# Kernel optimization log

Measured on AMD Instinct MI355X. Metric: run time of the kernel, lower is better.

The kernel has to match this reference:

```python
import jax, jax.numpy as jnp
import numpy as np

N_NODES = 100000
N_EDGES = 640000
IN_DIM = 128
HID_DIM = 256
N_CLASS = 40
K = 3  # propagation steps


def setup_inputs() -> dict:
    key = jax.random.key(0)
    ks = jax.random.split(key, 5)
    feats = jax.random.normal(ks[0], (N_NODES, IN_DIM), dtype=jnp.float32)
    src = jax.random.randint(ks[1], (N_EDGES,), 0, N_NODES, dtype=jnp.int32)
    dst = jax.random.randint(ks[2], (N_EDGES,), 0, N_NODES, dtype=jnp.int32)
    W1 = jax.random.normal(ks[3], (IN_DIM, HID_DIM), dtype=jnp.float32) * (1.0 / np.sqrt(IN_DIM))
    b1 = jnp.zeros((HID_DIM,), dtype=jnp.float32)
    W2 = jax.random.normal(ks[4], (HID_DIM, N_CLASS), dtype=jnp.float32) * (1.0 / np.sqrt(HID_DIM))
    b2 = jnp.zeros((N_CLASS,), dtype=jnp.float32)
    return {"feats": feats, "src": src, "dst": dst, "W1": W1, "b1": b1, "W2": W2, "b2": b2}


def _grand_conv(feats, src, dst, order):
    # symmetric normalization: norm = in_deg^{-1/2} (clamped at 1)
    deg = jax.ops.segment_sum(jnp.ones_like(dst, dtype=feats.dtype), dst, num_segments=N_NODES)
    norm = jnp.clip(deg, 1.0) ** -0.5  # [N]
    w = (norm[src] * norm[dst])[:, None]  # [E, 1] edge weights (u_mul_v)
    x = feats
    y = feats
    for _ in range(order):
        # u_mul_e gather-multiply, then scatter-sum into dst (SpMM)
        x = jax.ops.segment_sum(x[src] * w, dst, num_segments=N_NODES)
        y = y + x
    return y / (order + 1)


def reference(feats, src, dst, W1, b1, W2, b2):
    h = _grand_conv(feats, src, dst, K)           # [N, IN_DIM]
    h = jax.nn.relu(h @ W1 + b1)                  # [N, HID_DIM]
    logits = h @ W2 + b2                          # [N, N_CLASS]
    return jax.nn.log_softmax(logits, axis=-1)
```

## Files before the change

### kernel.cpp

```cpp
#include <hip/hip_runtime.h>

#define NN 100000
#define NE 640000
#define IND 128
#define HD 256
#define NC 40
#define MT 64
#define HPAD 264
#define LPAD 52
#define NB 196
#define CAP 5120
#define EPB 2500
#define SGRID 2048

typedef unsigned short u16;
typedef unsigned int u32;
typedef __attribute__((ext_vector_type(8))) short bf16x8;
typedef __attribute__((ext_vector_type(4))) float f32x4;

__device__ __forceinline__ float bf2f(u16 u) {
    union { u32 i; float f; } c; c.i = ((u32)u) << 16; return c.f;
}
__device__ __forceinline__ u16 f2bf(float f) {
    union { float f; u32 i; } c; c.f = f;
    u32 i = c.i;
    return (u16)((i + 0x7FFFu + ((i >> 16) & 1u)) >> 16);
}
__device__ __forceinline__ float rfl_f(float v) {
    return __int_as_float(__builtin_amdgcn_readfirstlane(__float_as_int(v)));
}
__device__ __forceinline__ int wave_incl_scan(int v, int lane) {
    #pragma unroll
    for (int off = 1; off < 64; off <<= 1) {
        int t = __shfl_up(v, off);
        if (lane >= off) v += t;
    }
    return v;
}

__global__ __launch_bounds__(256) void prep_k(
    const float* __restrict__ W1, const float* __restrict__ W2,
    u16* __restrict__ pw1, u16* __restrict__ pw2)
{
    const int gtid = blockIdx.x * 256 + threadIdx.x;
    if (gtid < 4096) {
        int lane = gtid & 63, fid = gtid >> 6;
        int ks = fid & 3, ct = fid >> 2;
        int quad = lane >> 4, m = lane & 15;
        int n = ct * 16 + m;
        u16* o = pw1 + (size_t)gtid * 8;
        #pragma unroll
        for (int j = 0; j < 8; j++) o[j] = f2bf(W1[(ks * 32 + quad * 8 + j) * HD + n]);
    } else if (gtid < 4096 + 1536) {
        int idx = gtid - 4096;
        int lane = idx & 63, fid = idx >> 6;
        int ks = fid & 7, ct = fid >> 3;
        int quad = lane >> 4, m = lane & 15;
        int n = ct * 16 + m;
        u16* o = pw2 + (size_t)idx * 8;
        #pragma unroll
        for (int j = 0; j < 8; j++)
            o[j] = (n < NC) ? f2bf(W2[(ks * 32 + quad * 8 + j) * NC + n]) : (u16)0;
    }
}

__global__ __launch_bounds__(256) void bin_k(
    const int* __restrict__ src, const int* __restrict__ dst,
    int* __restrict__ gcur, u32* __restrict__ ebuf)
{
    __shared__ int cnt[NB], cur[NB], rdest[NB];
    __shared__ u32 vals[EPB];
    const int tid = threadIdx.x;
    const int e0 = blockIdx.x * EPB;

    if (tid < NB) cnt[tid] = 0;
    __syncthreads();
    for (int i = tid; i < EPB; i += 256)
        atomicAdd(&cnt[dst[e0 + i] >> 9], 1);
    __syncthreads();
    if (tid < 64) {
        int carry = 0;
        #pragma unroll
        for (int c = 0; c < 4; c++) {
            const int idx = c * 64 + tid;
            const int v = (idx < NB) ? cnt[idx] : 0;
            const int incl = wave_incl_scan(v, tid);
            if (idx < NB) cur[idx] = carry + incl - v;
            carry += __shfl(incl, 63);
        }
    }
    __syncthreads();
    for (int i = tid; i < EPB; i += 256) {
        const int s = src[e0 + i], d = dst[e0 + i];
        const int b = d >> 9;
        const int slot = atomicAdd(&cur[b], 1);
        vals[slot] = ((u32)(d & 511) << 17) | (u32)s;
    }
    __syncthreads();
    if (tid < NB) {
        const int c = cnt[tid];
        int st = 0;
        if (c > 0) st = atomicAdd(&gcur[tid], c);
        rdest[tid] = (st + c <= CAP) ? st : -1;
    }
    __syncthreads();
    if (tid < NB) {
        const int c = cnt[tid];
        const int st = rdest[tid];
        if (c > 0 && st >= 0) {
            const int lo = cur[tid] - c;
            u32* o = ebuf + (size_t)tid * CAP + st;
            for (int k = 0; k < c; k++) o[k] = vals[lo + k];
        }
    }
}

__global__ __launch_bounds__(256) void build_k(
    const int* __restrict__ gcur, u32* __restrict__ ebuf,
    int2* __restrict__ rb, float* __restrict__ norm, float* __restrict__ invn)
{
    __shared__ int rowcnt[512], rowoff[512], csum[8];
    __shared__ u32 evals[CAP];
    const int tid = threadIdx.x;
    const int b = blockIdx.x;
    const int bB = b * CAP;
    const int r0 = b * 512;
    const int nb = min(__builtin_amdgcn_readfirstlane(gcur[b]), CAP);

    rowcnt[tid] = 0; rowcnt[256 + tid] = 0;
    __syncthreads();
    for (int i = tid; i < nb; i += 256) {
        const u32 v = ebuf[bB + i];
        evals[i] = v;
        atomicAdd(&rowcnt[(v >> 17) & 511], 1);
    }
    __syncthreads();
    {
        const int w = tid >> 6, lane = tid & 63;
        #pragma unroll
        for (int r = 0; r < 2; r++) {
            const int c = r * 4 + w;
            const int v = rowcnt[c * 64 + lane];
            const int incl = wave_incl_scan(v, lane);
            rowoff[c * 64 + lane] = incl - v;
            if (lane == 63) csum[c] = incl;
        }
        __syncthreads();
        if (tid == 0) {
            int run = 0;
            #pragma unroll
            for (int c = 0; c < 8; c++) { const int t = csum[c]; csum[c] = run; run += t; }
        }
        __syncthreads();
        #pragma unroll
        for (int r = 0; r < 2; r++) {
            const int c = r * 4 + w;
            rowoff[c * 64 + lane] += csum[c];
        }
    }
    __syncthreads();
    #pragma unroll
    for (int r = 0; r < 2; r++) {
        const int idx = r * 256 + tid;
        const int row = r0 + idx;
        if (row < NN) {
            const int deg = rowcnt[idx];
            const int base = bB + rowoff[idx];
            rb[row] = make_int2(base, base + deg);
            const float dc = fmaxf((float)deg, 1.0f);
            norm[row] = rsqrtf(dc);
            invn[row] = sqrtf(dc);
        }
    }
    __syncthreads();
    for (int i = tid; i < nb; i += 256) {
        const u32 v = evals[i];
        const int rl = (v >> 17) & 511;
        const int pos = atomicAdd(&rowoff[rl], 1);
        ebuf[bB + pos] = v & 0x1FFFFu;
    }
}

__global__ __launch_bounds__(256) void conv_k(
    const float4* __restrict__ feats4, const float* __restrict__ norm,
    uint2* __restrict__ zF2, uint2* __restrict__ zA2, uint2* __restrict__ zB2)
{
    const int gtid = blockIdx.x * 256 + threadIdx.x, gsz = gridDim.x * 256;
    if (gtid < 96) {
        const int which = gtid >> 5, idx = gtid & 31;
        uint2* b = (which == 0) ? zF2 : (which == 1) ? zA2 : zB2;
        b[(size_t)NN * 32 + idx] = make_uint2(0u, 0u);
    }
    for (int i = gtid; i < NN * (IND / 4); i += gsz) {
        const float4 v = feats4[i];
        const float n = norm[i >> 5];
        uint2 o;
        o.x = (u32)f2bf(v.x * n) | ((u32)f2bf(v.y * n) << 16);
        o.y = (u32)f2bf(v.z * n) | ((u32)f2bf(v.w * n) << 16);
        zF2[i] = o;
    }
}

template <int LAST>
__global__ __launch_bounds__(256) void spmm_k(
    const u32* __restrict__ x, u32* __restrict__ xnext,
    const u32* __restrict__ x0, const u32* __restrict__ x1,
    const int2* __restrict__ rb, const int* __restrict__ csr,
    const float* __restrict__ norm, const float* __restrict__ invn)
{
    const int lane = threadIdx.x & 63;
    int wid = (blockIdx.x * 256 + threadIdx.x) >> 6;
    wid = __builtin_amdgcn_readfirstlane(wid);
    const int nw = SGRID * 4;

    for (int row = wid; row < NN; row += nw) {
        const int2 be = rb[row];
        const int beg = __builtin_amdgcn_readfirstlane(be.x);
        const int end = __builtin_amdgcn_readfirstlane(be.y);
        const float n = rfl_f(norm[row]);

        float a0 = 0.f, a1 = 0.f;
        for (int b = beg; b < end; b += 8) {
            int sN[8];
            #pragma unroll
            for (int j = 0; j < 8; j++) {
                const int ee = b + j;
                const int c = csr[ee];
                int s = __builtin_amdgcn_readfirstlane(c);
                if (ee >= end) s = NN;
                sN[j] = s;
            }
            u32 u[8];
            #pragma unroll
            for (int j = 0; j < 8; j++) {
                const u32* rp = x + ((size_t)sN[j] << 6);
                u[j] = rp[lane];
            }
            #pragma unroll
            for (int j = 0; j < 8; j++) {
                a0 += __int_as_float((int)(u[j] << 16));
                a1 += __int_as_float((int)(u[j] & 0xFFFF0000u));
            }
        }

        const size_t ri = (size_t)row * 64 + lane;
        u32 o;
        if (!LAST) {
            const float n2 = n * n;
            o = (u32)f2bf(a0 * n2) | ((u32)f2bf(a1 * n2) << 16);
        } else {
            const float inv = rfl_f(invn[row]);
            const u32 v0 = x0[ri];
            const u32 v1 = x1[ri];
            const u32 v2 = x[ri];
            const float s0 = (bf2f((u16)(v0 & 0xFFFFu)) + bf2f((u16)(v1 & 0xFFFFu))
                            + bf2f((u16)(v2 & 0xFFFFu))) * inv + a0 * n;
            const float s1 = (bf2f((u16)(v0 >> 16)) + bf2f((u16)(v1 >> 16))
                            + bf2f((u16)(v2 >> 16))) * inv + a1 * n;
            o = (u32)f2bf(s0 * 0.25f) | ((u32)f2bf(s1 * 0.25f) << 16);
        }
        xnext[ri] = o;
    }
}

__global__ __launch_bounds__(256, 4) void mlp_mfma_k(
    const u16* __restrict__ ys, const u16* __restrict__ pw1,
    const float* __restrict__ B1, const u16* __restrict__ pw2,
    const float* __restrict__ B2, float* __restrict__ out, int N)
{
    __shared__ __align__(16) u16 h_s[MT * HPAD];
    const int t = threadIdx.x;
    const int w = t >> 6, lane = t & 63;
    const int quad = lane >> 4, m = lane & 15;
    const int node0 = blockIdx.x * MT;
    float* const lw = (float*)((char*)h_s + (size_t)w * 16 * HPAD * 2);

    bf16x8 av[4][4];
    #pragma unroll
    for (int g = 0; g < 4; g++) {
        int node = node0 + g * 16 + m;
        if (node > N - 1) node = N - 1;
        #pragma unroll
        for (int ks = 0; ks < 4; ks++)
            av[g][ks] = *(const bf16x8*)(ys + (size_t)node * IND + ks * 32 + quad * 8);
    }

    const u16* const pwl = pw1 + (size_t)lane * 8;
    const int ct0 = w * 4;
    bf16x8 wb[2][4];
    #pragma unroll
    for (int ks = 0; ks < 4; ks++)
        wb[0][ks] = *(const bf16x8*)(pwl + (size_t)((ct0 * 4 + ks) * 64) * 8);
    #pragma unroll
    for (int ct2 = 0; ct2 < 4; ct2++) {
        const int ct = ct0 + ct2;
        if (ct2 + 1 < 4) {
            #pragma unroll
            for (int ks = 0; ks < 4; ks++)
                wb[(ct2 + 1) & 1][ks] =
                    *(const bf16x8*)(pwl + (size_t)(((ct + 1) * 4 + ks) * 64) * 8);
        }
        const int cs = ct2 & 1;
        f32x4 acc[4];
        #pragma unroll
        for (int g = 0; g < 4; g++) acc[g] = (f32x4){ 0.f, 0.f, 0.f, 0.f };
        #pragma unroll
        for (int ks = 0; ks < 4; ks++) {
            #pragma unroll
            for (int g = 0; g < 4; g++)
                acc[g] = __builtin_amdgcn_mfma_f32_16x16x32_bf16(av[g][ks], wb[cs][ks], acc[g], 0, 0, 0);
        }
        const float b1c = B1[ct * 16 + m];
        #pragma unroll
        for (int g = 0; g < 4; g++) {
            #pragma unroll
            for (int r = 0; r < 4; r++) {
                const float hv = fmaxf(acc[g][r] + b1c, 0.0f);
                h_s[(g * 16 + quad * 4 + r) * HPAD + ct * 16 + m] = f2bf(hv);
            }
        }
    }
    __syncthreads();

    const u16* const pw2l = pw2 + (size_t)lane * 8;
    f32x4 acc2[3];
    #pragma unroll
    for (int ct = 0; ct < 3; ct++) acc2[ct] = (f32x4){ 0.f, 0.f, 0.f, 0.f };
    bf16x8 w2[3][3];
    #pragma unroll
    for (int ct = 0; ct < 3; ct++) {
        w2[0][ct] = *(const bf16x8*)(pw2l + (size_t)((ct * 8 + 0) * 64) * 8);
        w2[1][ct] = *(const bf16x8*)(pw2l + (size_t)((ct * 8 + 1) * 64) * 8);
    }
    #pragma unroll
    for (int ks = 0; ks < 8; ks++) {
        if (ks + 2 < 8) {
            const int ns = (ks + 2) % 3;
            #pragma unroll
            for (int ct = 0; ct < 3; ct++)
                w2[ns][ct] = *(const bf16x8*)(pw2l + (size_t)((ct * 8 + ks + 2) * 64) * 8);
        }
        const int cs = ks % 3;
        const bf16x8 a = *(const bf16x8*)&h_s[(w * 16 + m) * HPAD + ks * 32 + quad * 8];
        #pragma unroll
        for (int ct = 0; ct < 3; ct++)
            acc2[ct] = __builtin_amdgcn_mfma_f32_16x16x32_bf16(a, w2[cs][ct], acc2[ct], 0, 0, 0);
    }
    #pragma unroll
    for (int ct = 0; ct < 3; ct++) {
        const int cg = ct * 16 + m;
        const float b2c = (cg < NC) ? B2[cg] : 0.0f;
        #pragma unroll
        for (int r = 0; r < 4; r++)
            lw[(quad * 4 + r) * LPAD + cg] = acc2[ct][r] + b2c;
    }
    __syncthreads();

    if (t < MT) {
        const int node = node0 + t;
        if (node < N) {
            const float* ln = (const float*)((const char*)h_s + (size_t)(t >> 4) * 16 * HPAD * 2)
                              + (t & 15) * LPAD;
            float mx = -1e30f;
            #pragma unroll
            for (int c = 0; c < NC; c++) mx = fmaxf(mx, ln[c]);
            float s = 0.0f;
            #pragma unroll
            for (int c = 0; c < NC; c++) s += __expf(ln[c] - mx);
            const float lse = mx + __logf(s);
            float4* o = (float4*)(out + (size_t)node * NC);
            #pragma unroll
            for (int c4 = 0; c4 < NC / 4; c4++) {
                float4 v;
                v.x = ln[c4 * 4 + 0] - lse;
                v.y = ln[c4 * 4 + 1] - lse;
                v.z = ln[c4 * 4 + 2] - lse;
                v.w = ln[c4 * 4 + 3] - lse;
                o[c4] = v;
            }
        }
    }
}

extern "C" void kernel_launch(void* const* d_in, const int* in_sizes, int n_in,
                              void* d_out, int out_size, void* d_ws, size_t ws_size,
                              hipStream_t stream) {
    const float* feats = (const float*)d_in[0];
    const int* src = (const int*)d_in[1];
    const int* dst = (const int*)d_in[2];
    const float* W1 = (const float*)d_in[3];
    const float* B1 = (const float*)d_in[4];
    const float* W2 = (const float*)d_in[5];
    const float* B2 = (const float*)d_in[6];
    float* out = (float*)d_out;

    char* base = (char*)d_ws;
    size_t off = 0;
    auto alloc = [&](size_t bytes) -> void* {
        void* p = base + off;
        off += (bytes + 255) & ~(size_t)255;
        return p;
    };
    int*   gcur = (int*)  alloc((size_t)NB * 4);
    float* norm = (float*)alloc((size_t)NN * 4);
    float* invn = (float*)alloc((size_t)NN * 4);
    int2*  rb   = (int2*) alloc((size_t)NN * 8);
    u32*   ebuf = (u32*)  alloc(((size_t)NB * CAP + 64) * 4);
    u16*   pw1  = (u16*)  alloc((size_t)16 * 4 * 64 * 8 * 2);
    u16*   pw2  = (u16*)  alloc((size_t)3 * 8 * 64 * 8 * 2);
    u32*   zF   = (u32*)  alloc((size_t)(NN + 1) * (IND / 2) * 4);
    u32*   zA   = (u32*)  alloc((size_t)(NN + 1) * (IND / 2) * 4);
    u32*   zB   = (u32*)  alloc((size_t)(NN + 1) * (IND / 2) * 4);
    u32*   ys   = (u32*)  alloc((size_t)NN * (IND / 2) * 4);

    hipMemsetAsync(gcur, 0, 1024, stream);

    prep_k<<<22, 256, 0, stream>>>(W1, W2, pw1, pw2);
    bin_k<<<256, 256, 0, stream>>>(src, dst, gcur, ebuf);
    build_k<<<NB, 256, 0, stream>>>(gcur, ebuf, rb, norm, invn);
    conv_k<<<2048, 256, 0, stream>>>((const float4*)feats, norm,
                                     (uint2*)zF, (uint2*)zA, (uint2*)zB);

    spmm_k<0><<<SGRID, 256, 0, stream>>>(zF, zA, nullptr, nullptr, rb, (const int*)ebuf, norm, invn);
    spmm_k<0><<<SGRID, 256, 0, stream>>>(zA, zB, nullptr, nullptr, rb, (const int*)ebuf, norm, invn);
    spmm_k<1><<<SGRID, 256, 0, stream>>>(zB, ys, zF, zA, rb, (const int*)ebuf, norm, invn);

    const int mgrid = (NN + MT - 1) / MT;
    mlp_mfma_k<<<mgrid, 256, 0, stream>>>((const u16*)ys, pw1, B1, pw2, B2, out, NN);
}
```

Before: 247.0 us.

## Make MLP kernel persistent with LDS-resident weights and 128-node tiles

The MLP kernel becomes a persistent grid of 256 blocks with 512 threads each. Each block copies both packed weight matrices into shared memory once, then loops over 128-node tiles, reading weights from LDS instead of global memory. This removes repeated global weight fetches and most block launch overhead. The cost is heavy LDS use (about 157 KB per block), which likely allows only one block per CU. That lowers occupancy and leaves less room to hide the latency of the per-tile activation loads.

Result: slower. 255.5 us (+3.5%).

```diff
diff --git a/kernel.cpp b/kernel.cpp
--- a/kernel.cpp
+++ b/kernel.cpp
@@ -5,7 +5,7 @@
 #define IND 128
 #define HD 256
 #define NC 40
-#define MT 64
+#define MT2 128
 #define HPAD 264
 #define LPAD 52
 #define NB 196
@@ -263,122 +263,116 @@
     }
 }
 
-__global__ __launch_bounds__(256, 4) void mlp_mfma_k(
+__global__ __launch_bounds__(512, 2) void mlp_mfma_k(
     const u16* __restrict__ ys, const u16* __restrict__ pw1,
     const float* __restrict__ B1, const u16* __restrict__ pw2,
     const float* __restrict__ B2, float* __restrict__ out, int N)
 {
-    __shared__ __align__(16) u16 h_s[MT * HPAD];
+    __shared__ __align__(16) u16 w1s[16 * 4 * 64 * 8];
+    __shared__ __align__(16) u16 w2s[3 * 8 * 64 * 8];
+    __shared__ __align__(16) u16 h_s[MT2 * HPAD];
     const int t = threadIdx.x;
     const int w = t >> 6, lane = t & 63;
     const int quad = lane >> 4, m = lane & 15;
-    const int node0 = blockIdx.x * MT;
+    const int half = w >> 2;
+    const int ct0 = (w & 3) * 4;
     float* const lw = (float*)((char*)h_s + (size_t)w * 16 * HPAD * 2);
 
-    bf16x8 av[4][4];
-    #pragma unroll
-    for (int g = 0; g < 4; g++) {
-        int node = node0 + g * 16 + m;
-        if (node > N - 1) node = N - 1;
-        #pragma unroll
-        for (int ks = 0; ks < 4; ks++)
-            av[g][ks] = *(const bf16x8*)(ys + (size_t)node * IND + ks * 32 + quad * 8);
-    }
-
-    const u16* const pwl = pw1 + (size_t)lane * 8;
-    const int ct0 = w * 4;
-    bf16x8 wb[2][4];
-    #pragma unroll
-    for (int ks = 0; ks < 4; ks++)
-        wb[0][ks] = *(const bf16x8*)(pwl + (size_t)((ct0 * 4 + ks) * 64) * 8);
-    #pragma unroll
-    for (int ct2 = 0; ct2 < 4; ct2++) {
-        const int ct = ct0 + ct2;
-        if (ct2 + 1 < 4) {
+    {
+        const uint4* g1 = (const uint4*)pw1;  uint4* s1 = (uint4*)w1s;
+        #pragma unroll
+        for (int i = 0; i < 8; i++) s1[i * 512 + t] = g1[i * 512 + t];
+        const uint4* g2 = (const uint4*)pw2;  uint4* s2 = (uint4*)w2s;
+        #pragma unroll
+        for (int i = 0; i < 3; i++) s2[i * 512 + t] = g2[i * 512 + t];
+    }
+    __syncthreads();
+
+    const int ntiles = (N + MT2 - 1) / MT2;
+    for (int tb = blockIdx.x; tb < ntiles; tb += gridDim.x) {
+        const int node0 = tb * MT2 + half * 64;
+        bf16x8 av[4][4];
+        #pragma unroll
+        for (int g = 0; g < 4; g++) {
+            int node = node0 + g * 16 + m;
+            if (node > N - 1) node = N - 1;
             #pragma unroll
             for (int ks = 0; ks < 4; ks++)
-                wb[(ct2 + 1) & 1][ks] =
-                    *(const bf16x8*)(pwl + (size_t)(((ct + 1) * 4 + ks) * 64) * 8);
-        }
-        const int cs = ct2 & 1;
-        f32x4 acc[4];
-        #pragma unroll
-        for (int g = 0; g < 4; g++) acc[g] = (f32x4){ 0.f, 0.f, 0.f, 0.f };
-        #pragma unroll
-        for (int ks = 0; ks < 4; ks++) {
-            #pragma unroll
-            for (int g = 0; g < 4; g++)
-                acc[g] = __builtin_amdgcn_mfma_f32_16x16x32_bf16(av[g][ks], wb[cs][ks], acc[g], 0, 0, 0);
-        }
-        const float b1c = B1[ct * 16 + m];
-        #pragma unroll
-        for (int g = 0; g < 4; g++) {
-            #pragma unroll
-            for (int r = 0; r < 4; r++) {
-                const float hv = fmaxf(acc[g][r] + b1c, 0.0f);
-                h_s[(g * 16 + quad * 4 + r) * HPAD + ct * 16 + m] = f2bf(hv);
-            }
-        }
-    }
-    __syncthreads();
-
-    const u16* const pw2l = pw2 + (size_t)lane * 8;
-    f32x4 acc2[3];
-    #pragma unroll
-    for (int ct = 0; ct < 3; ct++) acc2[ct] = (f32x4){ 0.f, 0.f, 0.f, 0.f };
-    bf16x8 w2[3][3];
-    #pragma unroll
-    for (int ct = 0; ct < 3; ct++) {
-        w2[0][ct] = *(const bf16x8*)(pw2l + (size_t)((ct * 8 + 0) * 64) * 8);
-        w2[1][ct] = *(const bf16x8*)(pw2l + (size_t)((ct * 8 + 1) * 64) * 8);
-    }
-    #pragma unroll
-    for (int ks = 0; ks < 8; ks++) {
-        if (ks + 2 < 8) {
-            const int ns = (ks + 2) % 3;
-            #pragma unroll
-            for (int ct = 0; ct < 3; ct++)
-                w2[ns][ct] = *(const bf16x8*)(pw2l + (size_t)((ct * 8 + ks + 2) * 64) * 8);
-        }
-        const int cs = ks % 3;
-        const bf16x8 a = *(const bf16x8*)&h_s[(w * 16 + m) * HPAD + ks * 32 + quad * 8];
-        #pragma unroll
-        for (int ct = 0; ct < 3; ct++)
-            acc2[ct] = __builtin_amdgcn_mfma_f32_16x16x32_bf16(a, w2[cs][ct], acc2[ct], 0, 0, 0);
-    }
-    #pragma unroll
-    for (int ct = 0; ct < 3; ct++) {
-        const int cg = ct * 16 + m;
-        const float b2c = (cg < NC) ? B2[cg] : 0.0f;
-        #pragma unroll
-        for (int r = 0; r < 4; r++)
-            lw[(quad * 4 + r) * LPAD + cg] = acc2[ct][r] + b2c;
-    }
-    __syncthreads();
-
-    if (t < MT) {
-        const int node = node0 + t;
-        if (node < N) {
-            const float* ln = (const float*)((const char*)h_s + (size_t)(t >> 4) * 16 * HPAD * 2)
-                              + (t & 15) * LPAD;
-            float mx = -1e30f;
-            #pragma unroll
-            for (int c = 0; c < NC; c++) mx = fmaxf(mx, ln[c]);
-            float s = 0.0f;
-            #pragma unroll
-            for (int c = 0; c < NC; c++) s += __expf(ln[c] - mx);
-            const float lse = mx + __logf(s);
-            float4* o = (float4*)(out + (size_t)node * NC);
-            #pragma unroll
-            for (int c4 = 0; c4 < NC / 4; c4++) {
-                float4 v;
-                v.x = ln[c4 * 4 + 0] - lse;
-                v.y = ln[c4 * 4 + 1] - lse;
-                v.z = ln[c4 * 4 + 2] - lse;
-                v.w = ln[c4 * 4 + 3] - lse;
-                o[c4] = v;
-            }
-        }
+                av[g][ks] = *(const bf16x8*)(ys + (size_t)node * IND + ks * 32 + quad * 8);
+        }
+
+        #pragma unroll
+        for (int ct2 = 0; ct2 < 4; ct2++) {
+            const int ct = ct0 + ct2;
+            f32x4 acc[4];
+            #pragma unroll
+            for (int g = 0; g < 4; g++) acc[g] = (f32x4){ 0.f, 0.f, 0.f, 0.f };
+            #pragma unroll
+            for (int ks = 0; ks < 4; ks++) {
+                const bf16x8 b = *(const bf16x8*)&w1s[(size_t)((ct * 4 + ks) * 64 + lane) * 8];
+                #pragma unroll
+                for (int g = 0; g < 4; g++)
+                    acc[g] = __builtin_amdgcn_mfma_f32_16x16x32_bf16(av[g][ks], b, acc[g], 0, 0, 0);
+            }
+            const float b1c = B1[ct * 16 + m];
+            #pragma unroll
+            for (int g = 0; g < 4; g++) {
+                #pragma unroll
+                for (int r = 0; r < 4; r++) {
+                    const float hv = fmaxf(acc[g][r] + b1c, 0.0f);
+                    h_s[(half * 64 + g * 16 + quad * 4 + r) * HPAD + ct * 16 + m] = f2bf(hv);
+                }
+            }
+        }
+        __syncthreads();
+
+        f32x4 acc2[3];
+        #pragma unroll
+        for (int ct = 0; ct < 3; ct++) acc2[ct] = (f32x4){ 0.f, 0.f, 0.f, 0.f };
+        #pragma unroll
+        for (int ks = 0; ks < 8; ks++) {
+            const bf16x8 a = *(const bf16x8*)&h_s[(w * 16 + m) * HPAD + ks * 32 + quad * 8];
+            #pragma unroll
+            for (int ct = 0; ct < 3; ct++) {
+                const bf16x8 b = *(const bf16x8*)&w2s[(size_t)((ct * 8 + ks) * 64 + lane) * 8];
+                acc2[ct] = __builtin_amdgcn_mfma_f32_16x16x32_bf16(a, b, acc2[ct], 0, 0, 0);
+            }
+        }
+        #pragma unroll
+        for (int ct = 0; ct < 3; ct++) {
+            const int cg = ct * 16 + m;
+            const float b2c = (cg < NC) ? B2[cg] : 0.0f;
+            #pragma unroll
+            for (int r = 0; r < 4; r++)
+                lw[(quad * 4 + r) * LPAD + cg] = acc2[ct][r] + b2c;
+        }
+        __syncthreads();
+
+        if (t < MT2) {
+            const int node = tb * MT2 + t;
+            if (node < N) {
+                const float* ln = (const float*)((const char*)h_s + (size_t)(t >> 4) * 16 * HPAD * 2)
+                                  + (t & 15) * LPAD;
+                float mx = -1e30f;
+                #pragma unroll
+                for (int c = 0; c < NC; c++) mx = fmaxf(mx, ln[c]);
+                float s = 0.0f;
+                #pragma unroll
+                for (int c = 0; c < NC; c++) s += __expf(ln[c] - mx);
+                const float lse = mx + __logf(s);
+                float4* o = (float4*)(out + (size_t)node * NC);
+                #pragma unroll
+                for (int c4 = 0; c4 < NC / 4; c4++) {
+                    float4 v;
+                    v.x = ln[c4 * 4 + 0] - lse;
+                    v.y = ln[c4 * 4 + 1] - lse;
+                    v.z = ln[c4 * 4 + 2] - lse;
+                    v.w = ln[c4 * 4 + 3] - lse;
+                    o[c4] = v;
+                }
+            }
+        }
+        __syncthreads();
     }
 }
 
@@ -425,6 +419,5 @@
     spmm_k<0><<<SGRID, 256, 0, stream>>>(zA, zB, nullptr, nullptr, rb, (const int*)ebuf, norm, invn);
     spmm_k<1><<<SGRID, 256, 0, stream>>>(zB, ys, zF, zA, rb, (const int*)ebuf, norm, invn);
 
-    const int mgrid = (NN + MT - 1) / MT;
-    mlp_mfma_k<<<mgrid, 256, 0, stream>>>((const u16*)ys, pw1, B1, pw2, B2, out, NN);
-}
+    mlp_mfma_k<<<256, 512, 0, stream>>>((const u16*)ys, pw1, B1, pw2, B2, out, NN);
+}
```
